# Performance work log

Hardware: AMD Instinct MI355X
Metric: run time of the kernel (lower is better)

Reference implementation:

```python
import jax, jax.numpy as jnp
import numpy as np
from functools import partial

TAU = 2.0
BN_EPS = 1e-5
SG_ALPHA = 4.0  # spikingjelly surrogate.Sigmoid default

@jax.custom_vjp
def heaviside(x):
    return (x >= 0.0).astype(x.dtype)

def _heaviside_fwd(x):
    return heaviside(x), x

def _heaviside_bwd(x, g):
    s = jax.nn.sigmoid(SG_ALPHA * x)
    return (g * SG_ALPHA * s * (1.0 - s),)

heaviside.defvjp(_heaviside_fwd, _heaviside_bwd)

def lif(x_seq, v_threshold=1.0):
    # MultiStepLIFNode: tau=2, decay_input=True, v_reset=0 (hard reset), detach_reset
    def step(v, x):
        v = v + (x - v) / TAU
        s = heaviside(v - v_threshold)
        v = v * (1.0 - jax.lax.stop_gradient(s))
        return v, s
    _, s_seq = jax.lax.scan(step, jnp.zeros_like(x_seq[0]), x_seq)
    return s_seq

def conv1x1_bn(x, w, gamma, beta, mean, var, b=None):
    # x: [T,B,C,N]; w: [Cout,Cin]; 1x1 conv == channel matmul; BN in eval mode
    y = jnp.einsum('oc,tbcn->tbon', w, x)
    if b is not None:
        y = y + b[:, None]
    inv = gamma / jnp.sqrt(var + BN_EPS)
    return y * inv[:, None] + (beta - mean * inv)[:, None]

def setup_inputs() -> dict:
    key = jax.random.key(0)
    ks = jax.random.split(key, 24)
    T, B, C, N = 4, 32, 384, 196
    d = {}
    d['x'] = jax.random.normal(ks[0], (T, B, C, N), dtype=jnp.float32)
    d['policy'] = jax.random.uniform(ks[1], (T * B, N, 1), dtype=jnp.float32)
    scale = 1.0 / np.sqrt(C)
    for i, p in enumerate(['q', 'k', 'v', 'proj']):
        base = 2 + i * 5
        d[p + '_w'] = jax.random.normal(ks[base], (C, C), dtype=jnp.float32) * scale
        d[p + '_gamma'] = jnp.ones((C,), jnp.float32)
        d[p + '_beta'] = jnp.zeros((C,), jnp.float32)
        d[p + '_mean'] = jax.random.normal(ks[base + 1], (C,), dtype=jnp.float32) * 0.1
        d[p + '_var'] = jax.random.uniform(ks[base + 2], (C,), dtype=jnp.float32, minval=0.5, maxval=1.5)
    d['proj_b'] = jnp.zeros((C,), jnp.float32)
    return d

def _to_heads(s, H):
    T, B, C, N = s.shape
    # [T,B,C,N] -> [T,B,N,H,D] -> [T,B,H,N,D]
    return s.transpose(0, 1, 3, 2).reshape(T, B, N, H, C // H).transpose(0, 1, 3, 2, 4)

def reference(x, policy, q_w, q_gamma, q_beta, q_mean, q_var,
              k_w, k_gamma, k_beta, k_mean, k_var,
              v_w, v_gamma, v_beta, v_mean, v_var,
              proj_w, proj_gamma, proj_beta, proj_mean, proj_var, proj_b):
    T, B, C, N = x.shape
    H = 12
    attn_scale = 0.25
    q = _to_heads(lif(conv1x1_bn(x, q_w, q_gamma, q_beta, q_mean, q_var)), H)
    k = _to_heads(lif(conv1x1_bn(x, k_w, k_gamma, k_beta, k_mean, k_var)), H)
    v = _to_heads(lif(conv1x1_bn(x, v_w, v_gamma, v_beta, v_mean, v_var)), H)
    attn = jnp.einsum('tbhnd,tbhmd->tbhnm', q, k)
    # attention_policy: attn *= (policy + (1-policy)*eye)
    pol = policy.reshape(T, B, 1, 1, N)
    eye = jnp.eye(N, dtype=attn.dtype)
    attn = attn * (pol + (1.0 - pol) * eye)
    y = jnp.einsum('tbhnm,tbhmd->tbhnd', attn, v) * attn_scale
    y = y.transpose(0, 1, 2, 4, 3).reshape(T, B, C, N)
    y = lif(y, v_threshold=0.5)
    y = conv1x1_bn(y, proj_w, proj_gamma, proj_beta, proj_mean, proj_var, b=proj_b)
    return lif(y)
```

## Files before the change

kernel.cpp:

```cpp
#include <hip/hip_runtime.h>

typedef unsigned int u32;
typedef __bf16 bf16x8 __attribute__((ext_vector_type(8)));
typedef __bf16 bf16x4v __attribute__((ext_vector_type(4)));
typedef _Float16 f16x8 __attribute__((ext_vector_type(8)));
typedef float f32x4 __attribute__((ext_vector_type(4)));

#define Tn 4
#define Bn 32
#define Cn 384
#define Nn 196
#define Hn 12
#define CNn (Cn*Nn)
#define BCNn (Bn*CNn)
#define BHNn (Bn*Hn*Nn)
#define PBITS (Tn*BHNn)
#define TBCNn (Tn*BCNn)
#define NCOLS 6272
#define WSZ 147456

__device__ __forceinline__ void split3(float v, __bf16& h, __bf16& m, __bf16& l) {
  h = (__bf16)v;  float r = v - (float)h;
  m = (__bf16)r;  float r2 = r - (float)m;
  l = (__bf16)r2;
}
__device__ __forceinline__ void split2h(float v, _Float16& h, _Float16& l) {
  h = (_Float16)v;  l = (_Float16)(v - (float)h);
}

__device__ __forceinline__ void gl_lds16(const void* g, void* l) {
  __builtin_amdgcn_global_load_lds(
      (const __attribute__((address_space(1))) unsigned int*)g,
      (__attribute__((address_space(3))) unsigned int*)l, 16, 0, 0);
}

struct WSplitArgs {
  const float* w[4]; const float* g[4]; const float* be[4];
  const float* mu[4]; const float* va[4]; const float* bias;
};
__global__ __launch_bounds__(256) void prep(
    WSplitArgs a, _Float16* __restrict__ wsp16, __bf16* __restrict__ wspb,
    float* __restrict__ shv, const float* __restrict__ x,
    _Float16* __restrict__ xs) {
  __shared__ float tile[49 * 130];
  const int bx = blockIdx.x;
  const int tid = threadIdx.x;
  if (bx < 2304) {
    const int i = bx * 256 + tid;
    const int p = i / WSZ, r = i - p * WSZ;
    const int o = r / Cn;
    const float iv = a.g[p][o] / sqrtf(a.va[p][o] + 1e-5f);
    const float wv = a.w[p][r] * iv;
    if (p < 3) {
      _Float16 h, l;
      split2h(wv, h, l);
      wsp16[(size_t)(p * 2 + 0) * WSZ + r] = h;
      wsp16[(size_t)(p * 2 + 1) * WSZ + r] = l;
    } else {
      __bf16 h, m, l;
      split3(wv, h, m, l);
      wspb[(size_t)0 * WSZ + r] = h;
      wspb[(size_t)1 * WSZ + r] = m;
      wspb[(size_t)2 * WSZ + r] = l;
    }
    if (r - o * Cn == 0) {
      float sh = a.be[p][o] - a.mu[p][o] * iv;
      if (p == 3) sh += a.bias[o] * iv;
      shv[p * Cn + o] = sh;
    }
    return;
  }
  const int bid2 = bx - 2304;
  const int t = bid2 & 3, b = (bid2 >> 2) & 31, zz = bid2 >> 7;
  const int ct = zz >> 2, nch = zz & 3;
  const int c0 = ct * 128, n0 = nch * 49;
  for (int idx = tid; idx < 49 * 128; idx += 256) {
    const int n = idx % 49, c = idx / 49;
    tile[n * 130 + c] = x[(size_t)t * BCNn + (size_t)b * CNn +
                          (size_t)(c0 + c) * Nn + n0 + n];
  }
  __syncthreads();
  for (int idx = tid; idx < 49 * 64; idx += 256) {
    const int cp = idx & 63, n = idx >> 6;
    const float v0 = tile[n * 130 + cp * 2];
    const float v1 = tile[n * 130 + cp * 2 + 1];
    _Float16 h0, l0, h1, l1;
    split2h(v0, h0, l0);
    split2h(v1, h1, l1);
    const size_t col = (size_t)t * NCOLS + (size_t)b * Nn + n0 + n;
    union { _Float16 f[2]; u32 u; } uh, ul;
    uh.f[0] = h0; uh.f[1] = h1;
    ul.f[0] = l0; ul.f[1] = l1;
    ((u32*)(xs + col * Cn + c0))[cp] = uh.u;
    ((u32*)(xs + (size_t)TBCNn + col * Cn + c0))[cp] = ul.u;
  }
}

__global__ __launch_bounds__(256, 2) void gemm_qkv_lif(
    const _Float16* __restrict__ xs,
    const _Float16* __restrict__ wsp16,
    const float* __restrict__ shv,
    u32* __restrict__ bq, u32* __restrict__ bk, u32* __restrict__ bv)
{
  __shared__ _Float16 Asw[3][2][128][32];
  __shared__ _Float16 Bsw[3][2][64][32];
  const int orig = blockIdx.x;
  const int xcd = orig & 7, i8 = orig >> 3;
  const int wgid = xcd * 110 + (xcd < 2 ? xcd : 2) + i8;
  const int colt = wgid / 9, v = wgid - colt * 9;
  const int col0 = colt * 64;
  const int p = v / 3, mt = v - p * 3;
  const int o0 = mt * 128;
  const int tid = threadIdx.x, lane = tid & 63, wid = tid >> 6;
  const int wm = wid >> 1, wn = wid & 1;
  const int quad = lane >> 4, nl = lane & 15;
  u32* __restrict__ bits = (p == 0) ? bq : (p == 1) ? bk : bv;

  u32 aOff[4], bOff[2];
#pragma unroll
  for (int i = 0; i < 4; ++i) {
    const int c = i * 256 + wid * 64 + lane;
    const int s = c >> 9, row = (c >> 2) & 127, kb = c & 3;
    const int kbs = kb ^ ((row >> 1) & 3);
    aOff[i] = (u32)((((p * 2 + s) * WSZ) + (o0 + row) * Cn + kbs * 8) * 2);
  }
#pragma unroll
  for (int i = 0; i < 2; ++i) {
    const int c = i * 256 + wid * 64 + lane;
    const int s = c >> 8, rem = c & 255, row = rem >> 2, kb = rem & 3;
    const int kbs = kb ^ ((row >> 1) & 3);
    bOff[i] = (u32)(((size_t)s * TBCNn + (size_t)(col0 + row) * Cn + kbs * 8) * 2);
  }
  const char* wB = (const char*)wsp16;
  const char* xB = (const char*)xs;
  char* aD0 = (char*)&Asw[0][0][0][0] + wid * 1024;
  char* bD0 = (char*)&Bsw[0][0][0][0] + wid * 1024;

#define STAGE_A(ai_) do {                                                  \
    const u32 ak_ = (u32)(((ai_) % 12) * 64);                              \
    char* d_ = aD0 + ((ai_) % 3) * 16384;                                  \
    _Pragma("unroll") for (int i_ = 0; i_ < 4; ++i_)                       \
      gl_lds16(wB + aOff[i_] + ak_, d_ + i_ * 4096);                       \
  } while (0)
#define STAGE_B(g_) do {                                                   \
    const int t_ = ((g_) / 24) * 2 + ((g_) & 1);                           \
    const int kk_ = (((g_) % 24) >> 1);                                    \
    const u32 bk_ = (u32)(kk_ * 64) + (u32)t_ * (u32)(NCOLS * Cn * 2);     \
    char* d_ = bD0 + ((g_) % 3) * 8192;                                    \
    _Pragma("unroll") for (int i_ = 0; i_ < 2; ++i_)                       \
      gl_lds16(xB + bOff[i_] + bk_, d_ + i_ * 4096);                       \
  } while (0)

  f32x4 sh_[4];
#pragma unroll
  for (int mi = 0; mi < 4; ++mi)
    sh_[mi] = *(const f32x4*)&shv[p * Cn + o0 + wm * 64 + mi * 16 + quad * 4];

  f32x4 acc0[4][2], acc1[4][2];
  f32x4 vst[4][2] = {};

  auto epi = [&](f32x4 (&ac)[4][2], int t) {
#pragma unroll
    for (int ni = 0; ni < 2; ++ni) {
      u32 w0 = 0, w1 = 0;
#pragma unroll
      for (int mi = 0; mi < 4; ++mi) {
#pragma unroll
        for (int r = 0; r < 4; ++r) {
          const float y = ac[mi][ni][r] + sh_[mi][r];
          const float vv = vst[mi][ni][r];
          const float nv = vv + (y - vv) * 0.5f;
          const bool sk = nv >= 1.0f;
          vst[mi][ni][r] = sk ? 0.f : nv;
          const u32 b1 = sk ? 1u : 0u;
          const int pos = ((mi & 1) << 4) + (quad << 2) + r;
          if (mi < 2) w0 |= b1 << pos; else w1 |= b1 << pos;
        }
      }
      w0 |= __shfl_xor(w0, 16); w0 |= __shfl_xor(w0, 32);
      w1 |= __shfl_xor(w1, 16); w1 |= __shfl_xor(w1, 32);
      if (quad == 0) {
        const int col = col0 + wn * 32 + ni * 16 + nl;
        const int bb = col / Nn, nn = col - bb * Nn;
        u32* bp = bits + (size_t)t * BHNn +
                  ((size_t)bb * Hn + (mt * 4 + wm * 2)) * Nn + nn;
        bp[0] = w0;
        bp[Nn] = w1;
      }
    }
  };

  STAGE_B(0); STAGE_A(0); STAGE_B(1); STAGE_A(1);

#pragma unroll 1
  for (int gg = 0; gg < 24; ++gg) {
    const int abuf = gg % 3;
    const int be = (2 * gg) % 3, bo = (2 * gg + 1) % 3;
    const int kk = gg % 12;

    if (gg < 23) { asm volatile("s_waitcnt vmcnt(6)" ::: "memory"); }
    else         { asm volatile("s_waitcnt vmcnt(2)" ::: "memory"); }
    __builtin_amdgcn_s_barrier();
    __builtin_amdgcn_sched_barrier(0);
    if (gg < 23) STAGE_B(2 * gg + 2);
    if (kk == 0) {
#pragma unroll
      for (int mi = 0; mi < 4; ++mi)
#pragma unroll
        for (int ni = 0; ni < 2; ++ni) {
          acc0[mi][ni] = f32x4{0.f, 0.f, 0.f, 0.f};
          acc1[mi][ni] = f32x4{0.f, 0.f, 0.f, 0.f};
        }
    }
    f16x8 af0[4], af1[4];
#pragma unroll
    for (int mi = 0; mi < 4; ++mi) {
      const int ra = wm * 64 + mi * 16 + nl;
      const int ka = (quad ^ ((ra >> 1) & 3)) * 8;
      af0[mi] = *(const f16x8*)&Asw[abuf][0][ra][ka];
      af1[mi] = *(const f16x8*)&Asw[abuf][1][ra][ka];
    }
    {
      f16x8 bfr[2][2];
#pragma unroll
      for (int i = 0; i < 2; ++i) {
        const int rb = wn * 32 + i * 16 + nl;
        const int kb2 = (quad ^ ((rb >> 1) & 3)) * 8;
        bfr[0][i] = *(const f16x8*)&Bsw[be][0][rb][kb2];
        bfr[1][i] = *(const f16x8*)&Bsw[be][1][rb][kb2];
      }
      __builtin_amdgcn_s_setprio(1);
#pragma unroll
      for (int mi = 0; mi < 4; ++mi)
#pragma unroll
        for (int ni = 0; ni < 2; ++ni) {
          f32x4 c = acc0[mi][ni];
          c = __builtin_amdgcn_mfma_f32_16x16x32_f16(af0[mi], bfr[0][ni], c, 0, 0, 0);
          c = __builtin_amdgcn_mfma_f32_16x16x32_f16(af0[mi], bfr[1][ni], c, 0, 0, 0);
          c = __builtin_amdgcn_mfma_f32_16x16x32_f16(af1[mi], bfr[0][ni], c, 0, 0, 0);
          acc0[mi][ni] = c;
        }
      __builtin_amdgcn_s_setprio(0);
    }

    if (gg < 23) { asm volatile("s_waitcnt vmcnt(6)" ::: "memory"); }
    else         { asm volatile("s_waitcnt vmcnt(0)" ::: "memory"); }
    __builtin_amdgcn_s_barrier();
    __builtin_amdgcn_sched_barrier(0);
    if (gg < 23) STAGE_B(2 * gg + 3);
    if (gg < 22) STAGE_A(gg + 2);
    {
      f16x8 bfr[2][2];
#pragma unroll
      for (int i = 0; i < 2; ++i) {
        const int rb = wn * 32 + i * 16 + nl;
        const int kb2 = (quad ^ ((rb >> 1) & 3)) * 8;
        bfr[0][i] = *(const f16x8*)&Bsw[bo][0][rb][kb2];
        bfr[1][i] = *(const f16x8*)&Bsw[bo][1][rb][kb2];
      }
      __builtin_amdgcn_s_setprio(1);
#pragma unroll
      for (int mi = 0; mi < 4; ++mi)
#pragma unroll
        for (int ni = 0; ni < 2; ++ni) {
          f32x4 c = acc1[mi][ni];
          c = __builtin_amdgcn_mfma_f32_16x16x32_f16(af0[mi], bfr[0][ni], c, 0, 0, 0);
          c = __builtin_amdgcn_mfma_f32_16x16x32_f16(af0[mi], bfr[1][ni], c, 0, 0, 0);
          c = __builtin_amdgcn_mfma_f32_16x16x32_f16(af1[mi], bfr[0][ni], c, 0, 0, 0);
          acc1[mi][ni] = c;
        }
      __builtin_amdgcn_s_setprio(0);
    }
    if (kk == 11) {
      const int p2 = gg / 12;
      epi(acc0, p2 * 2 + 0);
      epi(acc1, p2 * 2 + 1);
    }
  }
#undef STAGE_A
#undef STAGE_B
}

#define ASTR 40
__global__ __launch_bounds__(256) void attn_lif(
    const u32* __restrict__ qb, const u32* __restrict__ kb,
    const u32* __restrict__ vb, const float* __restrict__ policy,
    __bf16* __restrict__ sp) {
  __shared__ u32 qs[208], ks[224], vs_[224];
  __shared__ float ps[224];
  __shared__ __bf16 psp[3][224];
  __shared__ __bf16 Al[112 * ASTR];
  __shared__ __bf16 Ul[3][32 * ASTR];
  const int blk = blockIdx.x;
  const int half = blk & 1;
  const int bh = blk >> 1;
  const int bN = bh / Hn;
  const int h = bh - bN * Hn;
  const int nbase = half * 112;
  const int ntiles = half ? 6 : 7;
  const int nrows = ntiles * 16;
  const int tid = threadIdx.x;
  const int lane = tid & 63, wid = tid >> 6;
  const int quad = lane >> 4, nl = lane & 15;
  const int arow = tid >> 1, ag = (tid & 1) << 4;

  float vst[2][2][4] = {};

  for (int t = 0; t < Tn; ++t) {
    const int tb = t * Bn + bN;
    const int gid = tb * Hn + h;
    if (t) __syncthreads();
    for (int i = tid; i < 224; i += 256) {
      const bool in = i < Nn;
      if (i < 208) qs[i] = in ? qb[(size_t)gid * Nn + i] : 0u;
      ks[i] = in ? kb[(size_t)gid * Nn + i] : 0u;
      vs_[i] = in ? vb[(size_t)gid * Nn + i] : 0u;
      const float p = in ? policy[(size_t)tb * Nn + i] : 0.f;
      ps[i] = p;
      __bf16 hh, mm, ll;
      split3(p, hh, mm, ll);
      psp[0][i] = hh; psp[1][i] = mm; psp[2][i] = ll;
    }
    __syncthreads();

    f32x4 acc[2][2] = {};

    for (int slab = 0; slab < 7; ++slab) {
      const int m0 = slab * 32;
      if (arow < nrows) {
        const u32 qn = qs[nbase + arow];
        __bf16 a16[16];
#pragma unroll
        for (int mk = 0; mk < 16; ++mk)
          a16[mk] = (__bf16)(float)__popc(qn & ks[m0 + ag + mk]);
        *(bf16x8*)&Al[arow * ASTR + ag] = *(bf16x8*)&a16[0];
        *(bf16x8*)&Al[arow * ASTR + ag + 8] = *(bf16x8*)&a16[8];
      }
      {
        const int dp = tid >> 3, mkg = (tid & 7) * 4;
        __bf16 u4[3][4];
#pragma unroll
        for (int j = 0; j < 4; ++j) {
          const int m = m0 + mkg + j;
          const bool bit = (vs_[m] >> dp) & 1u;
#pragma unroll
          for (int s = 0; s < 3; ++s)
            u4[s][j] = bit ? psp[s][m] : (__bf16)0.f;
        }
#pragma unroll
        for (int s = 0; s < 3; ++s)
          *(bf16x4v*)&Ul[s][dp * ASTR + mkg] = *(bf16x4v*)u4[s];
      }
      __syncthreads();
      bf16x8 bfr[3][2];
#pragma unroll
      for (int s = 0; s < 3; ++s)
#pragma unroll
        for (int nt = 0; nt < 2; ++nt)
          bfr[s][nt] = *(const bf16x8*)&Ul[s][(nt * 16 + nl) * ASTR + quad * 8];
#pragma unroll
      for (int mi = 0; mi < 2; ++mi) {
        const int lt = wid + mi * 4;
        if (lt < ntiles) {
          const bf16x8 af = *(const bf16x8*)&Al[(lt * 16 + nl) * ASTR + quad * 8];
#pragma unroll
          for (int nt = 0; nt < 2; ++nt) {
            f32x4 c = acc[mi][nt];
            c = __builtin_amdgcn_mfma_f32_16x16x32_bf16(af, bfr[0][nt], c, 0, 0, 0);
            c = __builtin_amdgcn_mfma_f32_16x16x32_bf16(af, bfr[1][nt], c, 0, 0, 0);
            c = __builtin_amdgcn_mfma_f32_16x16x32_bf16(af, bfr[2][nt], c, 0, 0, 0);
            acc[mi][nt] = c;
          }
        }
      }
      __syncthreads();
    }
#pragma unroll
    for (int mi = 0; mi < 2; ++mi) {
      const int lt = wid + mi * 4;
      if (lt >= ntiles) continue;
#pragma unroll
      for (int r = 0; r < 4; ++r) {
        const int n = nbase + lt * 16 + quad * 4 + r;
        if (n >= Nn) continue;
        const float ann = (float)__popc(qs[n] & ks[n]);
        const float wd = ann * (1.0f - ps[n]);
        const u32 vn = vs_[n];
        __bf16* op = sp + (size_t)t * BCNn + ((size_t)bN * Nn + n) * Cn + h * 32;
#pragma unroll
        for (int nt = 0; nt < 2; ++nt) {
          const int d = nt * 16 + nl;
          const float bit = (float)((vn >> d) & 1u);
          const float y = (acc[mi][nt][r] + wd * bit) * 0.25f;
          const float vv = vst[mi][nt][r];
          const float nv = vv + (y - vv) * 0.5f;
          const bool s = nv >= 0.5f;
          vst[mi][nt][r] = s ? 0.f : nv;
          op[d] = (__bf16)(s ? 1.0f : 0.0f);
        }
      }
    }
  }
}

__global__ __launch_bounds__(256, 3) void gemm_proj_lif(
    const __bf16* __restrict__ sp, const __bf16* __restrict__ wspb,
    const float* __restrict__ shv, float* __restrict__ out)
{
  __shared__ __bf16 Asw[3][3][64][32];
  __shared__ __bf16 Bsw[3][64][32];
  const int orig = blockIdx.x;
  const int xcd = orig & 7, i8 = orig >> 3;
  const int wgid = xcd * 73 + (xcd < 4 ? xcd : 4) + i8;
  const int colt = wgid / 6, ot = wgid - colt * 6;
  const int col0 = colt * 64;
  const int o0 = ot * 64;
  const int tid = threadIdx.x, lane = tid & 63, wid = tid >> 6;
  const int wm = wid >> 1, wn = wid & 1;
  const int quad = lane >> 4, nl = lane & 15;

  u32 aOff[3], bOff;
#pragma unroll
  for (int i = 0; i < 3; ++i) {
    const int c = i * 256 + wid * 64 + lane;
    const int s = c >> 8, rem = c & 255, row = rem >> 2, kb = rem & 3;
    const int kbs = kb ^ ((row >> 1) & 3);
    aOff[i] = (u32)(((s * WSZ) + (o0 + row) * Cn + kbs * 8) * 2);
  }
  {
    const int c = wid * 64 + lane;
    const int row = c >> 2, kb = c & 3;
    const int kbs = kb ^ ((row >> 1) & 3);
    bOff = (u32)(((size_t)(col0 + row) * Cn + kbs * 8) * 2);
  }
  const char* wB = (const char*)wspb;
  const char* sB = (const char*)sp;
  char* aD0 = (char*)&Asw[0][0][0][0] + wid * 1024;
  char* bD0 = (char*)&Bsw[0][0][0] + wid * 1024;

#define STAGE_A(ai_) do {                                                  \
    const u32 ak_ = (u32)(((ai_) % 12) * 64);                              \
    char* d_ = aD0 + ((ai_) % 3) * 12288;                                  \
    _Pragma("unroll") for (int i_ = 0; i_ < 3; ++i_)                       \
      gl_lds16(wB + aOff[i_] + ak_, d_ + i_ * 4096);                       \
  } while (0)
#define STAGE_B(g_) do {                                                   \
    const int t_ = ((g_) / 24) * 2 + ((g_) & 1);                           \
    const int kk_ = (((g_) % 24) >> 1);                                    \
    const u32 bk_ = (u32)(kk_ * 64) + (u32)t_ * (u32)(BCNn * 2);           \
    gl_lds16(sB + bOff + bk_, bD0 + ((g_) % 3) * 4096);                    \
  } while (0)

  f32x4 sh_[2];
#pragma unroll
  for (int mi = 0; mi < 2; ++mi)
    sh_[mi] = *(const f32x4*)&shv[3 * Cn + o0 + wm * 32 + mi * 16 + quad * 4];

  f32x4 acc0[2][2], acc1[2][2];
  f32x4 vst[2][2] = {};

  auto epi = [&](f32x4 (&ac)[2][2], int t) {
#pragma unroll
    for (int mi = 0; mi < 2; ++mi) {
      const int ob = o0 + wm * 32 + mi * 16 + quad * 4;
#pragma unroll
      for (int ni = 0; ni < 2; ++ni) {
        const int col = col0 + wn * 32 + ni * 16 + nl;
        const int bb = col / Nn, nn = col - bb * Nn;
        float* op = out + (size_t)t * BCNn + (size_t)bb * CNn + nn;
#pragma unroll
        for (int r = 0; r < 4; ++r) {
          const float y = ac[mi][ni][r] + sh_[mi][r];
          const float vv = vst[mi][ni][r];
          const float nv = vv + (y - vv) * 0.5f;
          const bool sk = nv >= 1.0f;
          vst[mi][ni][r] = sk ? 0.f : nv;
          op[(size_t)(ob + r) * Nn] = sk ? 1.0f : 0.0f;
        }
      }
    }
  };

  STAGE_B(0); STAGE_A(0); STAGE_B(1); STAGE_A(1);

#pragma unroll 1
  for (int gg = 0; gg < 24; ++gg) {
    const int abuf = gg % 3;
    const int be = (2 * gg) % 3, bo = (2 * gg + 1) % 3;
    const int kk = gg % 12;

    if (gg < 23) { asm volatile("s_waitcnt vmcnt(4)" ::: "memory"); }
    else         { asm volatile("s_waitcnt vmcnt(1)" ::: "memory"); }
    __builtin_amdgcn_s_barrier();
    __builtin_amdgcn_sched_barrier(0);
    if (gg < 23) STAGE_B(2 * gg + 2);
    if (kk == 0) {
#pragma unroll
      for (int mi = 0; mi < 2; ++mi)
#pragma unroll
        for (int ni = 0; ni < 2; ++ni) {
          acc0[mi][ni] = f32x4{0.f, 0.f, 0.f, 0.f};
          acc1[mi][ni] = f32x4{0.f, 0.f, 0.f, 0.f};
        }
    }
    bf16x8 af[3][2];
#pragma unroll
    for (int mi = 0; mi < 2; ++mi) {
      const int ra = wm * 32 + mi * 16 + nl;
      const int ka = (quad ^ ((ra >> 1) & 3)) * 8;
#pragma unroll
      for (int s = 0; s < 3; ++s)
        af[s][mi] = *(const bf16x8*)&Asw[abuf][s][ra][ka];
    }
    {
      bf16x8 bfr[2];
#pragma unroll
      for (int ni = 0; ni < 2; ++ni) {
        const int rb = wn * 32 + ni * 16 + nl;
        const int kb2 = (quad ^ ((rb >> 1) & 3)) * 8;
        bfr[ni] = *(const bf16x8*)&Bsw[be][rb][kb2];
      }
      __builtin_amdgcn_s_setprio(1);
#pragma unroll
      for (int mi = 0; mi < 2; ++mi)
#pragma unroll
        for (int ni = 0; ni < 2; ++ni) {
          f32x4 c = acc0[mi][ni];
          c = __builtin_amdgcn_mfma_f32_16x16x32_bf16(af[0][mi], bfr[ni], c, 0, 0, 0);
          c = __builtin_amdgcn_mfma_f32_16x16x32_bf16(af[1][mi], bfr[ni], c, 0, 0, 0);
          c = __builtin_amdgcn_mfma_f32_16x16x32_bf16(af[2][mi], bfr[ni], c, 0, 0, 0);
          acc0[mi][ni] = c;
        }
      __builtin_amdgcn_s_setprio(0);
    }

    if (gg < 23) { asm volatile("s_waitcnt vmcnt(4)" ::: "memory"); }
    else         { asm volatile("s_waitcnt vmcnt(0)" ::: "memory"); }
    __builtin_amdgcn_s_barrier();
    __builtin_amdgcn_sched_barrier(0);
    if (gg < 23) STAGE_B(2 * gg + 3);
    if (gg < 22) STAGE_A(gg + 2);
    {
      bf16x8 bfr[2];
#pragma unroll
      for (int ni = 0; ni < 2; ++ni) {
        const int rb = wn * 32 + ni * 16 + nl;
        const int kb2 = (quad ^ ((rb >> 1) & 3)) * 8;
        bfr[ni] = *(const bf16x8*)&Bsw[bo][rb][kb2];
      }
      __builtin_amdgcn_s_setprio(1);
#pragma unroll
      for (int mi = 0; mi < 2; ++mi)
#pragma unroll
        for (int ni = 0; ni < 2; ++ni) {
          f32x4 c = acc1[mi][ni];
          c = __builtin_amdgcn_mfma_f32_16x16x32_bf16(af[0][mi], bfr[ni], c, 0, 0, 0);
          c = __builtin_amdgcn_mfma_f32_16x16x32_bf16(af[1][mi], bfr[ni], c, 0, 0, 0);
          c = __builtin_amdgcn_mfma_f32_16x16x32_bf16(af[2][mi], bfr[ni], c, 0, 0, 0);
          acc1[mi][ni] = c;
        }
      __builtin_amdgcn_s_setprio(0);
    }
    if (kk == 11) {
      const int p2 = gg / 12;
      epi(acc0, p2 * 2 + 0);
      epi(acc1, p2 * 2 + 1);
    }
  }
#undef STAGE_A
#undef STAGE_B
}

extern "C" void kernel_launch(void* const* d_in, const int* in_sizes, int n_in,
                              void* d_out, int out_size, void* d_ws, size_t ws_size,
                              hipStream_t stream) {
  const float* x      = (const float*)d_in[0];
  const float* policy = (const float*)d_in[1];
  const float* qw = (const float*)d_in[2];
  const float* qg = (const float*)d_in[3];
  const float* qb_ = (const float*)d_in[4];
  const float* qm = (const float*)d_in[5];
  const float* qv = (const float*)d_in[6];
  const float* kw = (const float*)d_in[7];
  const float* kg = (const float*)d_in[8];
  const float* kbe = (const float*)d_in[9];
  const float* km = (const float*)d_in[10];
  const float* kv = (const float*)d_in[11];
  const float* vw = (const float*)d_in[12];
  const float* vg = (const float*)d_in[13];
  const float* vbe = (const float*)d_in[14];
  const float* vm = (const float*)d_in[15];
  const float* vv = (const float*)d_in[16];
  const float* pw = (const float*)d_in[17];
  const float* pg = (const float*)d_in[18];
  const float* pbe = (const float*)d_in[19];
  const float* pm = (const float*)d_in[20];
  const float* pv = (const float*)d_in[21];
  const float* pbias = (const float*)d_in[22];
  float* out = (float*)d_out;

  char* base = (char*)d_ws;
  _Float16* xs   = (_Float16*)base;
  _Float16* wsp16 = (_Float16*)(base + (size_t)TBCNn * 4);
  __bf16* wspb   = (__bf16*)((char*)wsp16 + (size_t)6 * WSZ * 2);
  float* shv     = (float*)((char*)wspb + (size_t)3 * WSZ * 2);
  u32* bq        = (u32*)((char*)shv + 4 * Cn * 4);
  u32* bk = bq + PBITS;
  u32* bv = bk + PBITS;
  __bf16* sp     = (__bf16*)(bv + PBITS);

  WSplitArgs wa;
  wa.w[0] = qw; wa.g[0] = qg; wa.be[0] = qb_; wa.mu[0] = qm; wa.va[0] = qv;
  wa.w[1] = kw; wa.g[1] = kg; wa.be[1] = kbe; wa.mu[1] = km; wa.va[1] = kv;
  wa.w[2] = vw; wa.g[2] = vg; wa.be[2] = vbe; wa.mu[2] = vm; wa.va[2] = vv;
  wa.w[3] = pw; wa.g[3] = pg; wa.be[3] = pbe; wa.mu[3] = pm; wa.va[3] = pv;
  wa.bias = pbias;
  prep<<<3840, 256, 0, stream>>>(wa, wsp16, wspb, shv, x, xs);

  gemm_qkv_lif<<<882, 256, 0, stream>>>(xs, wsp16, shv, bq, bk, bv);
  attn_lif<<<2 * Bn * Hn, 256, 0, stream>>>(bq, bk, bv, policy, sp);
  gemm_proj_lif<<<588, 256, 0, stream>>>(sp, wspb, shv, out);
}
```

Measured before the change: 299.6 us.

## Reassociate attention as Q·(Kᵀ·PV) to shrink per-head attention GEMM work

Rewrites the attention kernel to compute the small 32x32 product Kᵀ·(policy⊙V) first, then multiply Q by it, instead of building the full N×N popcount attention matrix. Each block now handles a whole head rather than half, which halves the grid and removes the per-slab popcount A-tile construction and most of the syncs. The intermediate is split into three bf16 parts to keep precision. The cost is an extra bf16 split and rounding step on the reassociated product, plus fewer blocks to spread across the device.

```diff
diff --git a/kernel.cpp b/kernel.cpp
--- a/kernel.cpp
+++ b/kernel.cpp
@@ -281,30 +281,27 @@
 #undef STAGE_B
 }
 
-#define ASTR 40
-__global__ __launch_bounds__(256) void attn_lif(
+#define USTR 232
+#define GSTR 40
+__global__ __launch_bounds__(256, 2) void attn_lif(
     const u32* __restrict__ qb, const u32* __restrict__ kb,
     const u32* __restrict__ vb, const float* __restrict__ policy,
     __bf16* __restrict__ sp) {
   __shared__ u32 qs[208], ks[224], vs_[224];
   __shared__ float ps[224];
   __shared__ __bf16 psp[3][224];
-  __shared__ __bf16 Al[112 * ASTR];
-  __shared__ __bf16 Ul[3][32 * ASTR];
-  const int blk = blockIdx.x;
-  const int half = blk & 1;
-  const int bh = blk >> 1;
+  __shared__ __bf16 Ul[3][32][USTR];
+  __shared__ __bf16 GT[3][32][GSTR];
+  const int bh = blockIdx.x;
   const int bN = bh / Hn;
   const int h = bh - bN * Hn;
-  const int nbase = half * 112;
-  const int ntiles = half ? 6 : 7;
-  const int nrows = ntiles * 16;
   const int tid = threadIdx.x;
   const int lane = tid & 63, wid = tid >> 6;
   const int quad = lane >> 4, nl = lane & 15;
-  const int arow = tid >> 1, ag = (tid & 1) << 4;
-
-  float vst[2][2][4] = {};
+  const int wm1 = wid >> 1, wn1 = wid & 1;
+  const __bf16 one = (__bf16)1.0f, zero = (__bf16)0.0f;
+
+  float vst[4][2][4] = {};
 
   for (int t = 0; t < Tn; ++t) {
     const int tb = t * Bn + bN;
@@ -323,65 +320,90 @@
     }
     __syncthreads();
 
-    f32x4 acc[2][2] = {};
-
+#pragma unroll
+    for (int it = 0; it < 7; ++it) {
+      const int idx = tid + it * 256;
+      const int d = idx & 31, mg = idx >> 5;
+      __bf16 u4[3][4];
+#pragma unroll
+      for (int j = 0; j < 4; ++j) {
+        const int m = mg * 4 + j;
+        const bool bit = (vs_[m] >> d) & 1u;
+#pragma unroll
+        for (int s = 0; s < 3; ++s)
+          u4[s][j] = bit ? psp[s][m] : zero;
+      }
+#pragma unroll
+      for (int s = 0; s < 3; ++s)
+        *(bf16x4v*)&Ul[s][d][mg * 4] = *(bf16x4v*)u4[s];
+    }
+    __syncthreads();
+
+    f32x4 gacc = {0.f, 0.f, 0.f, 0.f};
+    const int crow = wm1 * 16 + nl;
+    const int drow = wn1 * 16 + nl;
+#pragma unroll
     for (int slab = 0; slab < 7; ++slab) {
-      const int m0 = slab * 32;
-      if (arow < nrows) {
-        const u32 qn = qs[nbase + arow];
-        __bf16 a16[16];
-#pragma unroll
-        for (int mk = 0; mk < 16; ++mk)
-          a16[mk] = (__bf16)(float)__popc(qn & ks[m0 + ag + mk]);
-        *(bf16x8*)&Al[arow * ASTR + ag] = *(bf16x8*)&a16[0];
-        *(bf16x8*)&Al[arow * ASTR + ag + 8] = *(bf16x8*)&a16[8];
-      }
-      {
-        const int dp = tid >> 3, mkg = (tid & 7) * 4;
-        __bf16 u4[3][4];
-#pragma unroll
-        for (int j = 0; j < 4; ++j) {
-          const int m = m0 + mkg + j;
-          const bool bit = (vs_[m] >> dp) & 1u;
-#pragma unroll
-          for (int s = 0; s < 3; ++s)
-            u4[s][j] = bit ? psp[s][m] : (__bf16)0.f;
-        }
-#pragma unroll
-        for (int s = 0; s < 3; ++s)
-          *(bf16x4v*)&Ul[s][dp * ASTR + mkg] = *(bf16x4v*)u4[s];
-      }
-      __syncthreads();
-      bf16x8 bfr[3][2];
+      const int m0 = slab * 32 + quad * 8;
+      u32 kw[8];
+      *(uint4*)&kw[0] = *(const uint4*)&ks[m0];
+      *(uint4*)&kw[4] = *(const uint4*)&ks[m0 + 4];
+      __bf16 a8[8];
+#pragma unroll
+      for (int j = 0; j < 8; ++j)
+        a8[j] = ((kw[j] >> crow) & 1u) ? one : zero;
+      const bf16x8 af = *(const bf16x8*)a8;
 #pragma unroll
       for (int s = 0; s < 3; ++s)
-#pragma unroll
-        for (int nt = 0; nt < 2; ++nt)
-          bfr[s][nt] = *(const bf16x8*)&Ul[s][(nt * 16 + nl) * ASTR + quad * 8];
-#pragma unroll
-      for (int mi = 0; mi < 2; ++mi) {
-        const int lt = wid + mi * 4;
-        if (lt < ntiles) {
-          const bf16x8 af = *(const bf16x8*)&Al[(lt * 16 + nl) * ASTR + quad * 8];
-#pragma unroll
-          for (int nt = 0; nt < 2; ++nt) {
-            f32x4 c = acc[mi][nt];
-            c = __builtin_amdgcn_mfma_f32_16x16x32_bf16(af, bfr[0][nt], c, 0, 0, 0);
-            c = __builtin_amdgcn_mfma_f32_16x16x32_bf16(af, bfr[1][nt], c, 0, 0, 0);
-            c = __builtin_amdgcn_mfma_f32_16x16x32_bf16(af, bfr[2][nt], c, 0, 0, 0);
-            acc[mi][nt] = c;
-          }
-        }
-      }
-      __syncthreads();
-    }
-#pragma unroll
-    for (int mi = 0; mi < 2; ++mi) {
+        gacc = __builtin_amdgcn_mfma_f32_16x16x32_bf16(
+            af, *(const bf16x8*)&Ul[s][drow][slab * 32 + quad * 8], gacc, 0, 0, 0);
+    }
+#pragma unroll
+    for (int r = 0; r < 4; ++r) {
+      __bf16 gh, gm, gl;
+      split3(gacc[r], gh, gm, gl);
+      const int cc = wm1 * 16 + quad * 4 + r;
+      GT[0][drow][cc] = gh;
+      GT[1][drow][cc] = gm;
+      GT[2][drow][cc] = gl;
+    }
+    __syncthreads();
+
+    bf16x8 bfr2[3][2];
+#pragma unroll
+    for (int s = 0; s < 3; ++s)
+#pragma unroll
+      for (int nt = 0; nt < 2; ++nt)
+        bfr2[s][nt] = *(const bf16x8*)&GT[s][nt * 16 + nl][quad * 8];
+
+    f32x4 acc2[4][2] = {};
+#pragma unroll
+    for (int mi = 0; mi < 4; ++mi) {
       const int lt = wid + mi * 4;
-      if (lt >= ntiles) continue;
+      if (lt < 13) {
+        const u32 qw = qs[lt * 16 + nl];
+        __bf16 a8[8];
+#pragma unroll
+        for (int j = 0; j < 8; ++j)
+          a8[j] = ((qw >> (quad * 8 + j)) & 1u) ? one : zero;
+        const bf16x8 af2 = *(const bf16x8*)a8;
+#pragma unroll
+        for (int nt = 0; nt < 2; ++nt) {
+          f32x4 c = acc2[mi][nt];
+          c = __builtin_amdgcn_mfma_f32_16x16x32_bf16(af2, bfr2[0][nt], c, 0, 0, 0);
+          c = __builtin_amdgcn_mfma_f32_16x16x32_bf16(af2, bfr2[1][nt], c, 0, 0, 0);
+          c = __builtin_amdgcn_mfma_f32_16x16x32_bf16(af2, bfr2[2][nt], c, 0, 0, 0);
+          acc2[mi][nt] = c;
+        }
+      }
+    }
+#pragma unroll
+    for (int mi = 0; mi < 4; ++mi) {
+      const int lt = wid + mi * 4;
+      if (lt >= 13) continue;
 #pragma unroll
       for (int r = 0; r < 4; ++r) {
-        const int n = nbase + lt * 16 + quad * 4 + r;
+        const int n = lt * 16 + quad * 4 + r;
         if (n >= Nn) continue;
         const float ann = (float)__popc(qs[n] & ks[n]);
         const float wd = ann * (1.0f - ps[n]);
@@ -391,7 +413,7 @@
         for (int nt = 0; nt < 2; ++nt) {
           const int d = nt * 16 + nl;
           const float bit = (float)((vn >> d) & 1u);
-          const float y = (acc[mi][nt][r] + wd * bit) * 0.25f;
+          const float y = (acc2[mi][nt][r] + wd * bit) * 0.25f;
           const float vv = vst[mi][nt][r];
           const float nv = vv + (y - vv) * 0.5f;
           const bool s = nv >= 0.5f;
@@ -618,6 +640,6 @@
   prep<<<3840, 256, 0, stream>>>(wa, wsp16, wspb, shv, x, xs);
 
   gemm_qkv_lif<<<882, 256, 0, stream>>>(xs, wsp16, shv, bq, bk, bv);
-  attn_lif<<<2 * Bn * Hn, 256, 0, stream>>>(bq, bk, bv, policy, sp);
+  attn_lif<<<Bn * Hn, 256, 0, stream>>>(bq, bk, bv, policy, sp);
   gemm_proj_lif<<<588, 256, 0, stream>>>(sp, wspb, shv, out);
 }
```

Measured after the change: 283.5 us. 1.06x faster.
